# Performance work log

Hardware: AMD Instinct MI355X
Metric: run time of the kernel (lower is better)

The kernel has to match this reference:

```python
import jax, jax.numpy as jnp
import numpy as np

N_NODES = 100000
N_EDGES = 1600000
D_IN, D_HID, D_OUT = 64, 64, 40


def setup_inputs() -> dict:
    key = jax.random.key(0)
    ks = jax.random.split(key, 6)
    x = jax.random.normal(ks[0], (N_NODES, D_IN), dtype=jnp.float32)
    edge_index = jax.random.randint(ks[1], (2, N_EDGES), 0, N_NODES, dtype=jnp.int32)
    # Glorot-ish init for the two GCNConv linear weights
    W1 = jax.random.normal(ks[2], (D_IN, D_HID), dtype=jnp.float32) * (1.0 / np.sqrt(D_IN))
    b1 = jnp.zeros((D_HID,), dtype=jnp.float32)
    W2 = jax.random.normal(ks[3], (D_HID, D_OUT), dtype=jnp.float32) * (1.0 / np.sqrt(D_HID))
    b2 = jnp.zeros((D_OUT,), dtype=jnp.float32)
    return {"x": x, "edge_index": edge_index, "W1": W1, "b1": b1, "W2": W2, "b2": b2}


def reference(x, edge_index, W1, b1, W2, b2):
    N = x.shape[0]
    # GCNConv: add self-loops, symmetric normalization D^{-1/2}(A+I)D^{-1/2}
    loops = jnp.arange(N, dtype=edge_index.dtype)
    row = jnp.concatenate([edge_index[0], loops])  # source nodes (messages gathered here)
    col = jnp.concatenate([edge_index[1], loops])  # target nodes (scatter-add here)
    deg = jax.ops.segment_sum(jnp.ones_like(col, dtype=x.dtype), col, num_segments=N)
    dinv = jnp.where(deg > 0, jax.lax.rsqrt(deg), 0.0)
    norm = dinv[row] * dinv[col]  # [E+N]

    def gcn_conv(h, W, b):
        h = h @ W                                   # [N, d_out]
        msg = h[row] * norm[:, None]                # gather + scale  [E+N, d_out]
        return jax.ops.segment_sum(msg, col, num_segments=N) + b

    h = jax.nn.relu(gcn_conv(x, W1, b1))  # dropout is identity in eval mode
    logits = gcn_conv(h, W2, b2)
    return jax.nn.log_softmax(logits, axis=1)
```

## Files before the change

### kernel.cpp

```cpp
#include <hip/hip_runtime.h>
#include <hip/hip_bf16.h>
#include <math.h>

#define N_NODES 100000
#define N_EDGES 1600000
#define D_IN 64
#define D_HID 64
#define D_OUT 40
#define NBUCK 256
#define BSZ 391
#define BCAP 10240
#define P3_EPB 4096
#define P3_GRID ((N_EDGES + P3_EPB - 1) / P3_EPB)
#define GEMM_GRID ((N_NODES + 63) / 64)
#define AGG_GRID (N_NODES / 8)

typedef __hip_bfloat16 bf16;
typedef __attribute__((ext_vector_type(8))) short short8;
typedef __attribute__((ext_vector_type(4))) float f32x4;

__device__ __forceinline__ float bflo(unsigned int u) {
    union { unsigned int i; float f; } c; c.i = u << 16; return c.f;
}
__device__ __forceinline__ float bfhi(unsigned int u) {
    union { unsigned int i; float f; } c; c.i = u & 0xFFFF0000u; return c.f;
}
__device__ __forceinline__ unsigned short f2b(float f) {
    union { float f; unsigned int u; } c; c.f = f;
    unsigned int u = c.u + 0x7FFFu + ((c.u >> 16) & 1u);
    return (unsigned short)(u >> 16);
}
__device__ __forceinline__ float i8f(unsigned int w, int b) {
    return (float)((int)(w << ((3 - b) * 8)) >> 24);
}
__device__ __forceinline__ unsigned int qpack(float v0, float v1, float v2,
                                              float v3, float qs) {
    int q0 = __float2int_rn(v0 * qs), q1 = __float2int_rn(v1 * qs);
    int q2 = __float2int_rn(v2 * qs), q3 = __float2int_rn(v3 * qs);
    return (unsigned int)(q0 & 255) | ((unsigned int)(q1 & 255) << 8) |
           ((unsigned int)(q2 & 255) << 16) | ((unsigned int)(q3 & 255) << 24);
}

__global__ __launch_bounds__(256) void k_zero(int* __restrict__ p, int n) {
    int i = blockIdx.x * 256 + threadIdx.x;
    if (i < n) p[i] = 0;
}

__global__ __launch_bounds__(256) void k_place(const int* __restrict__ ei,
                                               int* __restrict__ fill_p,
                                               int* __restrict__ part) {
    __shared__ int cnt_l[NBUCK];
    __shared__ int base_l[NBUCK];
    cnt_l[threadIdx.x] = 0;
    __syncthreads();
    int e0 = blockIdx.x * P3_EPB;
    unsigned int meta[16];
#pragma unroll
    for (int k = 0; k < 16; k++) {
        int e = e0 + k * 256 + threadIdx.x;
        if (e < N_EDGES) {
            unsigned int c = (unsigned int)ei[N_EDGES + e];
            unsigned int b = c / 391u;
            unsigned int lc = c - b * 391u;
            unsigned int slot = atomicAdd(&cnt_l[b], 1);
            meta[k] = (b << 21) | (lc << 12) | slot;
        } else meta[k] = 0xFFFFFFFFu;
    }
    __syncthreads();
    int cv = cnt_l[threadIdx.x];
    if (cv) base_l[threadIdx.x] = threadIdx.x * BCAP +
                                  atomicAdd(&fill_p[threadIdx.x * 16], cv);
    __syncthreads();
#pragma unroll
    for (int k = 0; k < 16; k++) {
        if (meta[k] != 0xFFFFFFFFu) {
            int e = e0 + k * 256 + threadIdx.x;
            unsigned int b = meta[k] >> 21;
            unsigned int lc = (meta[k] >> 12) & 0x1FFu;
            unsigned int slot = meta[k] & 0xFFFu;
            unsigned int r = (unsigned int)ei[e];
            part[base_l[b] + slot] = (int)((lc << 17) | r);
        }
    }
}

__global__ __launch_bounds__(256) void k_build(const int* __restrict__ part,
                                               const int* __restrict__ fill_p,
                                               int* __restrict__ start,
                                               int* __restrict__ nkv,
                                               float* __restrict__ dinv,
                                               int* __restrict__ csr) {
    __shared__ int deg_l[392];
    __shared__ int excl_l[392];
    int tid = threadIdx.x;
    int b = blockIdx.x;
    int m = fill_p[b * 16];
    int base = b * BCAP;
    for (int i = tid; i < 392; i += 256) deg_l[i] = 0;
    __syncthreads();
    for (int i = tid; i < m; i += 256)
        atomicAdd(&deg_l[(unsigned int)part[base + i] >> 17], 1);
    __syncthreads();
    if (tid < 64) {
        int carry = 0;
        for (int ch = 0; ch < 7; ch++) {
            int idx = ch * 64 + tid;
            int val = (idx < 392) ? ((deg_l[idx] + 7) & ~7) : 0;
            int incl = val;
#pragma unroll
            for (int off = 1; off < 64; off <<= 1) {
                int u = __shfl_up(incl, off, 64);
                if (tid >= off) incl += u;
            }
            if (idx < 392) excl_l[idx] = carry + incl - val;
            carry += __shfl(incl, 63, 64);
        }
    }
    __syncthreads();
    int v0 = b * BSZ;
    for (int vl = tid; vl < BSZ; vl += 256) {
        int v = v0 + vl;
        if (v < N_NODES) {
            int d = deg_l[vl];
            start[v] = base + excl_l[vl];
            nkv[v] = (d + 7) >> 3;
            dinv[v] = rsqrtf((float)d + 1.0f);
        }
    }
    __syncthreads();
    for (int j = tid; j < 392 * 8; j += 256) {
        int vl = j >> 3, sl = j & 7;
        int d = deg_l[vl];
        int pc = ((d + 7) & ~7) - d;
        if (sl < pc) csr[base + excl_l[vl] + d + sl] = N_NODES;
    }
    __syncthreads();
    for (int i = tid; i < 392; i += 256) deg_l[i] = 0;
    __syncthreads();
    for (int i = tid; i < m; i += 256) {
        unsigned int p = (unsigned int)part[base + i];
        unsigned int lc = p >> 17;
        int s = atomicAdd(&deg_l[lc], 1);
        csr[base + excl_l[lc] + s] = (int)(p & 0x1FFFFu);
    }
}

__global__ __launch_bounds__(256) void k_prep(const float* __restrict__ W1,
                                              const float* __restrict__ W2,
                                              unsigned short* __restrict__ wp1,
                                              unsigned short* __restrict__ wp2,
                                              unsigned int* __restrict__ gb8,
                                              unsigned int* __restrict__ g2q,
                                              float* __restrict__ scale1,
                                              float* __restrict__ scale2) {
    int tid = threadIdx.x;
    if (tid < 16) gb8[(size_t)N_NODES * 16 + tid] = 0;
    else if (tid < 32) g2q[(size_t)N_NODES * 16 + (tid - 16)] = 0;
    else if (tid == 32) { scale1[N_NODES] = 0.f; scale2[N_NODES] = 0.f; }
    for (int i = tid; i < 4096; i += 256) {
        int e = i & 7, lane = (i >> 3) & 63, t = i >> 9;
        int kk = t >> 2, jt = t & 3;
        int row = kk * 32 + (lane >> 4) * 8 + e;
        int col = jt * 16 + (lane & 15);
        wp1[i] = f2b(W1[row * 64 + col]);
    }
    for (int i = tid; i < 3072; i += 256) {
        int e = i & 7, lane = (i >> 3) & 63, t = i >> 9;
        int kk = t / 3, jt = t - kk * 3;
        int row = kk * 32 + (lane >> 4) * 8 + e;
        int col = jt * 16 + (lane & 15);
        wp2[i] = (col < 40) ? f2b(W2[row * 40 + col]) : (unsigned short)0;
    }
}

__global__ __launch_bounds__(256) void k_gemm1m(const float* __restrict__ x,
                                                const short8* __restrict__ wp,
                                                const float* __restrict__ dinv,
                                                unsigned int* __restrict__ gb8,
                                                float* __restrict__ scale1) {
    int lane = threadIdx.x & 63;
    int wid = threadIdx.x >> 6;
    int node0 = (blockIdx.x * 4 + wid) * 16;
    if (node0 >= N_NODES) return;
    int vr = node0 + (lane & 15);
    if (vr >= N_NODES) vr = N_NODES - 1;
    int kg = lane >> 4;
    const float* px = x + (size_t)vr * 64 + kg * 8;
    short8 b0, b1;
    {
        float4 f0 = *(const float4*)px;
        float4 f1 = *(const float4*)(px + 4);
        b0[0] = (short)f2b(f0.x); b0[1] = (short)f2b(f0.y);
        b0[2] = (short)f2b(f0.z); b0[3] = (short)f2b(f0.w);
        b0[4] = (short)f2b(f1.x); b0[5] = (short)f2b(f1.y);
        b0[6] = (short)f2b(f1.z); b0[7] = (short)f2b(f1.w);
        float4 g0 = *(const float4*)(px + 32);
        float4 g1 = *(const float4*)(px + 36);
        b1[0] = (short)f2b(g0.x); b1[1] = (short)f2b(g0.y);
        b1[2] = (short)f2b(g0.z); b1[3] = (short)f2b(g0.w);
        b1[4] = (short)f2b(g1.x); b1[5] = (short)f2b(g1.y);
        b1[6] = (short)f2b(g1.z); b1[7] = (short)f2b(g1.w);
    }
    f32x4 acc[4];
#pragma unroll
    for (int jt = 0; jt < 4; jt++) acc[jt] = (f32x4){0.f, 0.f, 0.f, 0.f};
#pragma unroll
    for (int jt = 0; jt < 4; jt++) {
        acc[jt] = __builtin_amdgcn_mfma_f32_16x16x32_bf16(
            wp[(0 * 4 + jt) * 64 + lane], b0, acc[jt], 0, 0, 0);
        acc[jt] = __builtin_amdgcn_mfma_f32_16x16x32_bf16(
            wp[(1 * 4 + jt) * 64 + lane], b1, acc[jt], 0, 0, 0);
    }
    float d = dinv[vr];
    float mv[4][4];
    float amax = 0.f;
#pragma unroll
    for (int jt = 0; jt < 4; jt++)
#pragma unroll
        for (int i = 0; i < 4; i++) {
            float val = acc[jt][i] * d;
            mv[jt][i] = val;
            amax = fmaxf(amax, fabsf(val));
        }
    amax = fmaxf(amax, __shfl_xor(amax, 16, 64));
    amax = fmaxf(amax, __shfl_xor(amax, 32, 64));
    float qs = (amax > 0.f) ? 127.f / amax : 0.f;
    if (kg == 0) scale1[vr] = amax * (1.f / 127.f);
    unsigned int* gp = gb8 + (size_t)vr * 16 + kg;
#pragma unroll
    for (int jt = 0; jt < 4; jt++)
        gp[jt * 4] = qpack(mv[jt][0], mv[jt][1], mv[jt][2], mv[jt][3], qs);
}

__global__ __launch_bounds__(256) void k_gemm2m(const unsigned short* __restrict__ hb,
                                                const short8* __restrict__ wp,
                                                const float* __restrict__ dinv,
                                                unsigned int* __restrict__ g2q,
                                                float* __restrict__ scale2) {
    int lane = threadIdx.x & 63;
    int wid = threadIdx.x >> 6;
    int node0 = (blockIdx.x * 4 + wid) * 16;
    if (node0 >= N_NODES) return;
    int vr = node0 + (lane & 15);
    if (vr >= N_NODES) vr = N_NODES - 1;
    int kg = lane >> 4;
    const short8* h8 = (const short8*)hb;
    short8 b0 = h8[(size_t)vr * 8 + kg];
    short8 b1 = h8[(size_t)vr * 8 + 4 + kg];
    f32x4 acc[3];
#pragma unroll
    for (int jt = 0; jt < 3; jt++) acc[jt] = (f32x4){0.f, 0.f, 0.f, 0.f};
#pragma unroll
    for (int jt = 0; jt < 3; jt++) {
        acc[jt] = __builtin_amdgcn_mfma_f32_16x16x32_bf16(
            wp[(0 * 3 + jt) * 64 + lane], b0, acc[jt], 0, 0, 0);
        acc[jt] = __builtin_amdgcn_mfma_f32_16x16x32_bf16(
            wp[(1 * 3 + jt) * 64 + lane], b1, acc[jt], 0, 0, 0);
    }
    float d = dinv[vr];
    bool v2 = (kg < 2);
    float mv[3][4];
    float amax = 0.f;
#pragma unroll
    for (int jt = 0; jt < 3; jt++)
#pragma unroll
        for (int i = 0; i < 4; i++) {
            float val = acc[jt][i] * d;
            mv[jt][i] = val;
            if (jt < 2 || v2) amax = fmaxf(amax, fabsf(val));
        }
    amax = fmaxf(amax, __shfl_xor(amax, 16, 64));
    amax = fmaxf(amax, __shfl_xor(amax, 32, 64));
    float qs = (amax > 0.f) ? 127.f / amax : 0.f;
    if (kg == 0) scale2[vr] = amax * (1.f / 127.f);
    unsigned int* gp = g2q + (size_t)vr * 16;
    gp[0 * 4 + kg] = qpack(mv[0][0], mv[0][1], mv[0][2], mv[0][3], qs);
    gp[1 * 4 + kg] = qpack(mv[1][0], mv[1][1], mv[1][2], mv[1][3], qs);
    gp[8 + kg] = v2 ? qpack(mv[2][0], mv[2][1], mv[2][2], mv[2][3], qs) : 0u;
    gp[12 + kg] = 0u;
}

__global__ __launch_bounds__(256) void k_agg1(const int* __restrict__ csr,
                                              const int* __restrict__ start,
                                              const int* __restrict__ nkv,
                                              const unsigned int* __restrict__ gb8,
                                              const float* __restrict__ scale1,
                                              const float* __restrict__ dinv,
                                              const float* __restrict__ b1,
                                              unsigned short* __restrict__ hb) {
    int lane = threadIdx.x & 63;
    int g = lane >> 3;
    int lq = lane & 7;
    int v0 = (blockIdx.x * 4 + (threadIdx.x >> 6)) * 2;
    int v1 = v0 + 1;
    int s0 = start[v0] + g, s1 = start[v1] + g;
    int n0 = nkv[v0], n1 = nkv[v1];
    float a0=0.f,a1=0.f,a2=0.f,a3=0.f,a4=0.f,a5=0.f,a6=0.f,a7=0.f;
    float c0=0.f,c1=0.f,c2=0.f,c3=0.f,c4=0.f,c5=0.f,c6=0.f,c7=0.f;
    if (g == 0) {
        float sA = scale1[v0];
        uint2 uA = *(const uint2*)(gb8 + (size_t)v0 * 16 + lq * 2);
        a0 = fmaf(i8f(uA.x,0), sA, a0); a1 = fmaf(i8f(uA.x,1), sA, a1);
        a2 = fmaf(i8f(uA.x,2), sA, a2); a3 = fmaf(i8f(uA.x,3), sA, a3);
        a4 = fmaf(i8f(uA.y,0), sA, a4); a5 = fmaf(i8f(uA.y,1), sA, a5);
        a6 = fmaf(i8f(uA.y,2), sA, a6); a7 = fmaf(i8f(uA.y,3), sA, a7);
        float sB = scale1[v1];
        uint2 uB = *(const uint2*)(gb8 + (size_t)v1 * 16 + lq * 2);
        c0 = fmaf(i8f(uB.x,0), sB, c0); c1 = fmaf(i8f(uB.x,1), sB, c1);
        c2 = fmaf(i8f(uB.x,2), sB, c2); c3 = fmaf(i8f(uB.x,3), sB, c3);
        c4 = fmaf(i8f(uB.y,0), sB, c4); c5 = fmaf(i8f(uB.y,1), sB, c5);
        c6 = fmaf(i8f(uB.y,2), sB, c6); c7 = fmaf(i8f(uB.y,3), sB, c7);
    }
    int nc = (n0 < n1) ? n0 : n1;
#pragma unroll 2
    for (int k = 0; k < nc; k++) {
        int r0 = csr[s0 + k * 8];
        int r1 = csr[s1 + k * 8];
        float sA = scale1[r0], sB = scale1[r1];
        uint2 uA = *(const uint2*)(gb8 + (size_t)r0 * 16 + lq * 2);
        uint2 uB = *(const uint2*)(gb8 + (size_t)r1 * 16 + lq * 2);
        a0 = fmaf(i8f(uA.x,0), sA, a0); a1 = fmaf(i8f(uA.x,1), sA, a1);
        a2 = fmaf(i8f(uA.x,2), sA, a2); a3 = fmaf(i8f(uA.x,3), sA, a3);
        a4 = fmaf(i8f(uA.y,0), sA, a4); a5 = fmaf(i8f(uA.y,1), sA, a5);
        a6 = fmaf(i8f(uA.y,2), sA, a6); a7 = fmaf(i8f(uA.y,3), sA, a7);
        c0 = fmaf(i8f(uB.x,0), sB, c0); c1 = fmaf(i8f(uB.x,1), sB, c1);
        c2 = fmaf(i8f(uB.x,2), sB, c2); c3 = fmaf(i8f(uB.x,3), sB, c3);
        c4 = fmaf(i8f(uB.y,0), sB, c4); c5 = fmaf(i8f(uB.y,1), sB, c5);
        c6 = fmaf(i8f(uB.y,2), sB, c6); c7 = fmaf(i8f(uB.y,3), sB, c7);
    }
    for (int k = nc; k < n0; k++) {
        int r = csr[s0 + k * 8];
        float sc = scale1[r];
        uint2 u = *(const uint2*)(gb8 + (size_t)r * 16 + lq * 2);
        a0 = fmaf(i8f(u.x,0), sc, a0); a1 = fmaf(i8f(u.x,1), sc, a1);
        a2 = fmaf(i8f(u.x,2), sc, a2); a3 = fmaf(i8f(u.x,3), sc, a3);
        a4 = fmaf(i8f(u.y,0), sc, a4); a5 = fmaf(i8f(u.y,1), sc, a5);
        a6 = fmaf(i8f(u.y,2), sc, a6); a7 = fmaf(i8f(u.y,3), sc, a7);
    }
    for (int k = nc; k < n1; k++) {
        int r = csr[s1 + k * 8];
        float sc = scale1[r];
        uint2 u = *(const uint2*)(gb8 + (size_t)r * 16 + lq * 2);
        c0 = fmaf(i8f(u.x,0), sc, c0); c1 = fmaf(i8f(u.x,1), sc, c1);
        c2 = fmaf(i8f(u.x,2), sc, c2); c3 = fmaf(i8f(u.x,3), sc, c3);
        c4 = fmaf(i8f(u.y,0), sc, c4); c5 = fmaf(i8f(u.y,1), sc, c5);
        c6 = fmaf(i8f(u.y,2), sc, c6); c7 = fmaf(i8f(u.y,3), sc, c7);
    }
#pragma unroll
    for (int o = 8; o < 64; o <<= 1) {
        a0 += __shfl_xor(a0, o, 64); a1 += __shfl_xor(a1, o, 64);
        a2 += __shfl_xor(a2, o, 64); a3 += __shfl_xor(a3, o, 64);
        a4 += __shfl_xor(a4, o, 64); a5 += __shfl_xor(a5, o, 64);
        a6 += __shfl_xor(a6, o, 64); a7 += __shfl_xor(a7, o, 64);
        c0 += __shfl_xor(c0, o, 64); c1 += __shfl_xor(c1, o, 64);
        c2 += __shfl_xor(c2, o, 64); c3 += __shfl_xor(c3, o, 64);
        c4 += __shfl_xor(c4, o, 64); c5 += __shfl_xor(c5, o, 64);
        c6 += __shfl_xor(c6, o, 64); c7 += __shfl_xor(c7, o, 64);
    }
    bool hi = (lane >= 32);
    int v = hi ? v1 : v0;
    float d = dinv[v];
    float e0 = hi ? c0 : a0, e1 = hi ? c1 : a1, e2 = hi ? c2 : a2;
    float e3 = hi ? c3 : a3, e4 = hi ? c4 : a4, e5 = hi ? c5 : a5;
    float e6 = hi ? c6 : a6, e7 = hi ? c7 : a7;
    float4 bb0 = ((const float4*)b1)[lq * 2];
    float4 bb1 = ((const float4*)b1)[lq * 2 + 1];
    float h0 = fmaxf(d * e0 + bb0.x, 0.f), h1 = fmaxf(d * e1 + bb0.y, 0.f);
    float h2 = fmaxf(d * e2 + bb0.z, 0.f), h3 = fmaxf(d * e3 + bb0.w, 0.f);
    float h4 = fmaxf(d * e4 + bb1.x, 0.f), h5 = fmaxf(d * e5 + bb1.y, 0.f);
    float h6 = fmaxf(d * e6 + bb1.z, 0.f), h7 = fmaxf(d * e7 + bb1.w, 0.f);
    if (g == 0 || g == 4) {
        uint4 o;
        o.x = (unsigned int)f2b(h0) | ((unsigned int)f2b(h1) << 16);
        o.y = (unsigned int)f2b(h2) | ((unsigned int)f2b(h3) << 16);
        o.z = (unsigned int)f2b(h4) | ((unsigned int)f2b(h5) << 16);
        o.w = (unsigned int)f2b(h6) | ((unsigned int)f2b(h7) << 16);
        *(uint4*)(hb + (size_t)v * 64 + lq * 8) = o;
    }
}

__global__ __launch_bounds__(256) void k_agg2(const int* __restrict__ csr,
                                              const int* __restrict__ start,
                                              const int* __restrict__ nkv,
                                              const unsigned int* __restrict__ g2q,
                                              const float* __restrict__ scale2,
                                              const float* __restrict__ dinv,
                                              const float* __restrict__ b2v,
                                              float* __restrict__ out) {
    int lane = threadIdx.x & 63;
    int g = lane >> 3;
    int lq = lane & 7;
    int v0 = (blockIdx.x * 4 + (threadIdx.x >> 6)) * 2;
    int v1 = v0 + 1;
    int s0 = start[v0] + g, s1 = start[v1] + g;
    int n0 = nkv[v0], n1 = nkv[v1];
    float a0=0.f,a1=0.f,a2=0.f,a3=0.f,a4=0.f,a5=0.f,a6=0.f,a7=0.f;
    float c0=0.f,c1=0.f,c2=0.f,c3=0.f,c4=0.f,c5=0.f,c6=0.f,c7=0.f;
    if (g == 0) {
        float sA = scale2[v0];
        uint2 uA = *(const uint2*)(g2q + (size_t)v0 * 16 + lq * 2);
        a0 = fmaf(i8f(uA.x,0), sA, a0); a1 = fmaf(i8f(uA.x,1), sA, a1);
        a2 = fmaf(i8f(uA.x,2), sA, a2); a3 = fmaf(i8f(uA.x,3), sA, a3);
        a4 = fmaf(i8f(uA.y,0), sA, a4); a5 = fmaf(i8f(uA.y,1), sA, a5);
        a6 = fmaf(i8f(uA.y,2), sA, a6); a7 = fmaf(i8f(uA.y,3), sA, a7);
        float sB = scale2[v1];
        uint2 uB = *(const uint2*)(g2q + (size_t)v1 * 16 + lq * 2);
        c0 = fmaf(i8f(uB.x,0), sB, c0); c1 = fmaf(i8f(uB.x,1), sB, c1);
        c2 = fmaf(i8f(uB.x,2), sB, c2); c3 = fmaf(i8f(uB.x,3), sB, c3);
        c4 = fmaf(i8f(uB.y,0), sB, c4); c5 = fmaf(i8f(uB.y,1), sB, c5);
        c6 = fmaf(i8f(uB.y,2), sB, c6); c7 = fmaf(i8f(uB.y,3), sB, c7);
    }
    int nc = (n0 < n1) ? n0 : n1;
#pragma unroll 2
    for (int k = 0; k < nc; k++) {
        int r0 = csr[s0 + k * 8];
        int r1 = csr[s1 + k * 8];
        float sA = scale2[r0], sB = scale2[r1];
        uint2 uA = *(const uint2*)(g2q + (size_t)r0 * 16 + lq * 2);
        uint2 uB = *(const uint2*)(g2q + (size_t)r1 * 16 + lq * 2);
        a0 = fmaf(i8f(uA.x,0), sA, a0); a1 = fmaf(i8f(uA.x,1), sA, a1);
        a2 = fmaf(i8f(uA.x,2), sA, a2); a3 = fmaf(i8f(uA.x,3), sA, a3);
        a4 = fmaf(i8f(uA.y,0), sA, a4); a5 = fmaf(i8f(uA.y,1), sA, a5);
        a6 = fmaf(i8f(uA.y,2), sA, a6); a7 = fmaf(i8f(uA.y,3), sA, a7);
        c0 = fmaf(i8f(uB.x,0), sB, c0); c1 = fmaf(i8f(uB.x,1), sB, c1);
        c2 = fmaf(i8f(uB.x,2), sB, c2); c3 = fmaf(i8f(uB.x,3), sB, c3);
        c4 = fmaf(i8f(uB.y,0), sB, c4); c5 = fmaf(i8f(uB.y,1), sB, c5);
        c6 = fmaf(i8f(uB.y,2), sB, c6); c7 = fmaf(i8f(uB.y,3), sB, c7);
    }
    for (int k = nc; k < n0; k++) {
        int r = csr[s0 + k * 8];
        float sc = scale2[r];
        uint2 u = *(const uint2*)(g2q + (size_t)r * 16 + lq * 2);
        a0 = fmaf(i8f(u.x,0), sc, a0); a1 = fmaf(i8f(u.x,1), sc, a1);
        a2 = fmaf(i8f(u.x,2), sc, a2); a3 = fmaf(i8f(u.x,3), sc, a3);
        a4 = fmaf(i8f(u.y,0), sc, a4); a5 = fmaf(i8f(u.y,1), sc, a5);
        a6 = fmaf(i8f(u.y,2), sc, a6); a7 = fmaf(i8f(u.y,3), sc, a7);
    }
    for (int k = nc; k < n1; k++) {
        int r = csr[s1 + k * 8];
        float sc = scale2[r];
        uint2 u = *(const uint2*)(g2q + (size_t)r * 16 + lq * 2);
        c0 = fmaf(i8f(u.x,0), sc, c0); c1 = fmaf(i8f(u.x,1), sc, c1);
        c2 = fmaf(i8f(u.x,2), sc, c2); c3 = fmaf(i8f(u.x,3), sc, c3);
        c4 = fmaf(i8f(u.y,0), sc, c4); c5 = fmaf(i8f(u.y,1), sc, c5);
        c6 = fmaf(i8f(u.y,2), sc, c6); c7 = fmaf(i8f(u.y,3), sc, c7);
    }
#pragma unroll
    for (int o = 8; o < 64; o <<= 1) {
        a0 += __shfl_xor(a0, o, 64); a1 += __shfl_xor(a1, o, 64);
        a2 += __shfl_xor(a2, o, 64); a3 += __shfl_xor(a3, o, 64);
        a4 += __shfl_xor(a4, o, 64); a5 += __shfl_xor(a5, o, 64);
        a6 += __shfl_xor(a6, o, 64); a7 += __shfl_xor(a7, o, 64);
        c0 += __shfl_xor(c0, o, 64); c1 += __shfl_xor(c1, o, 64);
        c2 += __shfl_xor(c2, o, 64); c3 += __shfl_xor(c3, o, 64);
        c4 += __shfl_xor(c4, o, 64); c5 += __shfl_xor(c5, o, 64);
        c6 += __shfl_xor(c6, o, 64); c7 += __shfl_xor(c7, o, 64);
    }
    bool hi = (lane >= 32);
    int v = hi ? v1 : v0;
    float d = dinv[v];
    float e0 = hi ? c0 : a0, e1 = hi ? c1 : a1, e2 = hi ? c2 : a2;
    float e3 = hi ? c3 : a3, e4 = hi ? c4 : a4, e5 = hi ? c5 : a5;
    float e6 = hi ? c6 : a6, e7 = hi ? c7 : a7;
    bool act = (lq < 5);
    float4 bb0 = act ? ((const float4*)b2v)[lq * 2] : make_float4(0.f,0.f,0.f,0.f);
    float4 bb1 = act ? ((const float4*)b2v)[lq * 2 + 1] : make_float4(0.f,0.f,0.f,0.f);
    float l0 = act ? d * e0 + bb0.x : -INFINITY;
    float l1 = act ? d * e1 + bb0.y : -INFINITY;
    float l2 = act ? d * e2 + bb0.z : -INFINITY;
    float l3 = act ? d * e3 + bb0.w : -INFINITY;
    float l4 = act ? d * e4 + bb1.x : -INFINITY;
    float l5 = act ? d * e5 + bb1.y : -INFINITY;
    float l6 = act ? d * e6 + bb1.z : -INFINITY;
    float l7 = act ? d * e7 + bb1.w : -INFINITY;
    float m = fmaxf(fmaxf(fmaxf(l0, l1), fmaxf(l2, l3)),
                    fmaxf(fmaxf(l4, l5), fmaxf(l6, l7)));
#pragma unroll
    for (int o = 1; o < 8; o <<= 1) m = fmaxf(m, __shfl_xor(m, o, 64));
    float ex = act ? (__expf(l0 - m) + __expf(l1 - m) + __expf(l2 - m) +
                      __expf(l3 - m) + __expf(l4 - m) + __expf(l5 - m) +
                      __expf(l6 - m) + __expf(l7 - m)) : 0.f;
#pragma unroll
    for (int o = 1; o < 8; o <<= 1) ex += __shfl_xor(ex, o, 64);
    float lse = m + logf(ex);
    if ((g == 0 || g == 4) && act) {
        float* op = out + (size_t)v * 40 + lq * 8;
        *(float4*)op = make_float4(l0 - lse, l1 - lse, l2 - lse, l3 - lse);
        *(float4*)(op + 4) = make_float4(l4 - lse, l5 - lse, l6 - lse, l7 - lse);
    }
}

extern "C" void kernel_launch(void* const* d_in, const int* in_sizes, int n_in,
                              void* d_out, int out_size, void* d_ws, size_t ws_size,
                              hipStream_t stream) {
    const float* x  = (const float*)d_in[0];
    const int*   ei = (const int*)d_in[1];
    const float* W1 = (const float*)d_in[2];
    const float* b1 = (const float*)d_in[3];
    const float* W2 = (const float*)d_in[4];
    const float* b2 = (const float*)d_in[5];
    float* out = (float*)d_out;

    const int N = N_NODES;
    int*   part  = (int*)d_ws;
    int*   csr   = part + NBUCK * BCAP;
    int*   start = csr + NBUCK * BCAP;
    int*   nkv   = start + N;
    int*   fill  = nkv + N;
    float* dinv  = (float*)(fill + 4096);
    float* scale1 = dinv + N;
    float* scale2 = scale1 + N + 4;
    unsigned short* hb  = (unsigned short*)(scale2 + N + 4);
    unsigned int* gb8 = (unsigned int*)(hb + (size_t)N * 64);
    unsigned int* g2q = gb8 + (size_t)(N + 1) * 16;
    unsigned short* wp1 = (unsigned short*)(g2q + (size_t)(N + 1) * 16);
    unsigned short* wp2 = wp1 + 4096;

    k_zero<<<16, 256, 0, stream>>>(fill, 4096);
    k_prep<<<1, 256, 0, stream>>>(W1, W2, wp1, wp2, gb8, g2q, scale1, scale2);
    k_place<<<P3_GRID, 256, 0, stream>>>(ei, fill, part);
    k_build<<<NBUCK, 256, 0, stream>>>(part, fill, start, nkv, dinv, csr);
    k_gemm1m<<<GEMM_GRID, 256, 0, stream>>>(x, (const short8*)wp1, dinv, gb8, scale1);
    k_agg1<<<AGG_GRID, 256, 0, stream>>>(csr, start, nkv, gb8, scale1, dinv, b1, hb);
    k_gemm2m<<<GEMM_GRID, 256, 0, stream>>>(hb, (const short8*)wp2, dinv, g2q, scale2);
    k_agg2<<<AGG_GRID, 256, 0, stream>>>(csr, start, nkv, g2q, scale2, dinv, b2, out);
}
```

Baseline: 239.7 us.

## Replace per-node int8 quantized messages with fp16 messages in aggregation

Switches the gathered per-node feature buffers from int8 with a per-node float scale to packed fp16 values. Aggregation now accumulates them with fdot2 instead of sign-extend plus fma, which drops the separate scale lookups and the amax reduction in the GEMM epilogues. The cost is twice the bytes per gathered row (128B for layer 1, 80B for layer 2), so the random gathers move more traffic. The bucket capacity is also reduced, shrinking the workspace.

```diff
diff --git a/kernel.cpp b/kernel.cpp
--- a/kernel.cpp
+++ b/kernel.cpp
@@ -9,7 +9,7 @@
 #define D_OUT 40
 #define NBUCK 256
 #define BSZ 391
-#define BCAP 10240
+#define BCAP 8192
 #define P3_EPB 4096
 #define P3_GRID ((N_EDGES + P3_EPB - 1) / P3_EPB)
 #define GEMM_GRID ((N_NODES + 63) / 64)
@@ -18,27 +18,32 @@
 typedef __hip_bfloat16 bf16;
 typedef __attribute__((ext_vector_type(8))) short short8;
 typedef __attribute__((ext_vector_type(4))) float f32x4;
-
-__device__ __forceinline__ float bflo(unsigned int u) {
-    union { unsigned int i; float f; } c; c.i = u << 16; return c.f;
-}
-__device__ __forceinline__ float bfhi(unsigned int u) {
-    union { unsigned int i; float f; } c; c.i = u & 0xFFFF0000u; return c.f;
-}
+typedef __attribute__((ext_vector_type(2))) _Float16 h2f;
+typedef __attribute__((ext_vector_type(2))) __fp16 fp16x2;
+
 __device__ __forceinline__ unsigned short f2b(float f) {
     union { float f; unsigned int u; } c; c.f = f;
     unsigned int u = c.u + 0x7FFFu + ((c.u >> 16) & 1u);
     return (unsigned short)(u >> 16);
 }
-__device__ __forceinline__ float i8f(unsigned int w, int b) {
-    return (float)((int)(w << ((3 - b) * 8)) >> 24);
-}
-__device__ __forceinline__ unsigned int qpack(float v0, float v1, float v2,
-                                              float v3, float qs) {
-    int q0 = __float2int_rn(v0 * qs), q1 = __float2int_rn(v1 * qs);
-    int q2 = __float2int_rn(v2 * qs), q3 = __float2int_rn(v3 * qs);
-    return (unsigned int)(q0 & 255) | ((unsigned int)(q1 & 255) << 8) |
-           ((unsigned int)(q2 & 255) << 16) | ((unsigned int)(q3 & 255) << 24);
+__device__ __forceinline__ unsigned int pkh(float a, float b) {
+#if __has_builtin(__builtin_amdgcn_cvt_pkrtz)
+    union { fp16x2 h; unsigned int u; } c;
+    c.h = __builtin_amdgcn_cvt_pkrtz(a, b);
+    return c.u;
+#else
+    union { _Float16 h[2]; unsigned int u; } c;
+    c.h[0] = (_Float16)a; c.h[1] = (_Float16)b; return c.u;
+#endif
+}
+__device__ __forceinline__ void acc2(unsigned int w, float& e, float& o) {
+    union { unsigned int u; h2f h; } c; c.u = w;
+#if __has_builtin(__builtin_amdgcn_fdot2)
+    e = __builtin_amdgcn_fdot2(c.h, (h2f){(_Float16)1.f, (_Float16)0.f}, e, false);
+    o = __builtin_amdgcn_fdot2(c.h, (h2f){(_Float16)0.f, (_Float16)1.f}, o, false);
+#else
+    e += (float)c.h[0]; o += (float)c.h[1];
+#endif
 }
 
 __global__ __launch_bounds__(256) void k_zero(int* __restrict__ p, int n) {
@@ -149,14 +154,11 @@
                                               const float* __restrict__ W2,
                                               unsigned short* __restrict__ wp1,
                                               unsigned short* __restrict__ wp2,
-                                              unsigned int* __restrict__ gb8,
-                                              unsigned int* __restrict__ g2q,
-                                              float* __restrict__ scale1,
-                                              float* __restrict__ scale2) {
+                                              unsigned int* __restrict__ gbh,
+                                              unsigned int* __restrict__ g2h) {
     int tid = threadIdx.x;
-    if (tid < 16) gb8[(size_t)N_NODES * 16 + tid] = 0;
-    else if (tid < 32) g2q[(size_t)N_NODES * 16 + (tid - 16)] = 0;
-    else if (tid == 32) { scale1[N_NODES] = 0.f; scale2[N_NODES] = 0.f; }
+    if (tid < 32) gbh[(size_t)N_NODES * 32 + tid] = 0;
+    else if (tid < 52) g2h[(size_t)N_NODES * 20 + (tid - 32)] = 0;
     for (int i = tid; i < 4096; i += 256) {
         int e = i & 7, lane = (i >> 3) & 63, t = i >> 9;
         int kk = t >> 2, jt = t & 3;
@@ -176,8 +178,7 @@
 __global__ __launch_bounds__(256) void k_gemm1m(const float* __restrict__ x,
                                                 const short8* __restrict__ wp,
                                                 const float* __restrict__ dinv,
-                                                unsigned int* __restrict__ gb8,
-                                                float* __restrict__ scale1) {
+                                                unsigned short* __restrict__ gbh) {
     int lane = threadIdx.x & 63;
     int wid = threadIdx.x >> 6;
     int node0 = (blockIdx.x * 4 + wid) * 16;
@@ -212,31 +213,20 @@
             wp[(1 * 4 + jt) * 64 + lane], b1, acc[jt], 0, 0, 0);
     }
     float d = dinv[vr];
-    float mv[4][4];
-    float amax = 0.f;
-#pragma unroll
-    for (int jt = 0; jt < 4; jt++)
-#pragma unroll
-        for (int i = 0; i < 4; i++) {
-            float val = acc[jt][i] * d;
-            mv[jt][i] = val;
-            amax = fmaxf(amax, fabsf(val));
-        }
-    amax = fmaxf(amax, __shfl_xor(amax, 16, 64));
-    amax = fmaxf(amax, __shfl_xor(amax, 32, 64));
-    float qs = (amax > 0.f) ? 127.f / amax : 0.f;
-    if (kg == 0) scale1[vr] = amax * (1.f / 127.f);
-    unsigned int* gp = gb8 + (size_t)vr * 16 + kg;
-#pragma unroll
-    for (int jt = 0; jt < 4; jt++)
-        gp[jt * 4] = qpack(mv[jt][0], mv[jt][1], mv[jt][2], mv[jt][3], qs);
+    unsigned short* gp = gbh + (size_t)vr * 64 + kg * 4;
+#pragma unroll
+    for (int jt = 0; jt < 4; jt++) {
+        uint2 w;
+        w.x = pkh(acc[jt][0] * d, acc[jt][1] * d);
+        w.y = pkh(acc[jt][2] * d, acc[jt][3] * d);
+        *(uint2*)(gp + jt * 16) = w;
+    }
 }
 
 __global__ __launch_bounds__(256) void k_gemm2m(const unsigned short* __restrict__ hb,
                                                 const short8* __restrict__ wp,
                                                 const float* __restrict__ dinv,
-                                                unsigned int* __restrict__ g2q,
-                                                float* __restrict__ scale2) {
+                                                unsigned short* __restrict__ g2h) {
     int lane = threadIdx.x & 63;
     int wid = threadIdx.x >> 6;
     int node0 = (blockIdx.x * 4 + wid) * 16;
@@ -258,33 +248,26 @@
             wp[(1 * 3 + jt) * 64 + lane], b1, acc[jt], 0, 0, 0);
     }
     float d = dinv[vr];
-    bool v2 = (kg < 2);
-    float mv[3][4];
-    float amax = 0.f;
-#pragma unroll
-    for (int jt = 0; jt < 3; jt++)
-#pragma unroll
-        for (int i = 0; i < 4; i++) {
-            float val = acc[jt][i] * d;
-            mv[jt][i] = val;
-            if (jt < 2 || v2) amax = fmaxf(amax, fabsf(val));
-        }
-    amax = fmaxf(amax, __shfl_xor(amax, 16, 64));
-    amax = fmaxf(amax, __shfl_xor(amax, 32, 64));
-    float qs = (amax > 0.f) ? 127.f / amax : 0.f;
-    if (kg == 0) scale2[vr] = amax * (1.f / 127.f);
-    unsigned int* gp = g2q + (size_t)vr * 16;
-    gp[0 * 4 + kg] = qpack(mv[0][0], mv[0][1], mv[0][2], mv[0][3], qs);
-    gp[1 * 4 + kg] = qpack(mv[1][0], mv[1][1], mv[1][2], mv[1][3], qs);
-    gp[8 + kg] = v2 ? qpack(mv[2][0], mv[2][1], mv[2][2], mv[2][3], qs) : 0u;
-    gp[12 + kg] = 0u;
+    unsigned short* gp = g2h + (size_t)vr * 40;
+#pragma unroll
+    for (int jt = 0; jt < 2; jt++) {
+        uint2 w;
+        w.x = pkh(acc[jt][0] * d, acc[jt][1] * d);
+        w.y = pkh(acc[jt][2] * d, acc[jt][3] * d);
+        *(uint2*)(gp + jt * 16 + kg * 4) = w;
+    }
+    if (kg < 2) {
+        uint2 w;
+        w.x = pkh(acc[2][0] * d, acc[2][1] * d);
+        w.y = pkh(acc[2][2] * d, acc[2][3] * d);
+        *(uint2*)(gp + 32 + kg * 4) = w;
+    }
 }
 
 __global__ __launch_bounds__(256) void k_agg1(const int* __restrict__ csr,
                                               const int* __restrict__ start,
                                               const int* __restrict__ nkv,
-                                              const unsigned int* __restrict__ gb8,
-                                              const float* __restrict__ scale1,
+                                              const unsigned int* __restrict__ gbh,
                                               const float* __restrict__ dinv,
                                               const float* __restrict__ b1,
                                               unsigned short* __restrict__ hb) {
@@ -298,53 +281,36 @@
     float a0=0.f,a1=0.f,a2=0.f,a3=0.f,a4=0.f,a5=0.f,a6=0.f,a7=0.f;
     float c0=0.f,c1=0.f,c2=0.f,c3=0.f,c4=0.f,c5=0.f,c6=0.f,c7=0.f;
     if (g == 0) {
-        float sA = scale1[v0];
-        uint2 uA = *(const uint2*)(gb8 + (size_t)v0 * 16 + lq * 2);
-        a0 = fmaf(i8f(uA.x,0), sA, a0); a1 = fmaf(i8f(uA.x,1), sA, a1);
-        a2 = fmaf(i8f(uA.x,2), sA, a2); a3 = fmaf(i8f(uA.x,3), sA, a3);
-        a4 = fmaf(i8f(uA.y,0), sA, a4); a5 = fmaf(i8f(uA.y,1), sA, a5);
-        a6 = fmaf(i8f(uA.y,2), sA, a6); a7 = fmaf(i8f(uA.y,3), sA, a7);
-        float sB = scale1[v1];
-        uint2 uB = *(const uint2*)(gb8 + (size_t)v1 * 16 + lq * 2);
-        c0 = fmaf(i8f(uB.x,0), sB, c0); c1 = fmaf(i8f(uB.x,1), sB, c1);
-        c2 = fmaf(i8f(uB.x,2), sB, c2); c3 = fmaf(i8f(uB.x,3), sB, c3);
-        c4 = fmaf(i8f(uB.y,0), sB, c4); c5 = fmaf(i8f(uB.y,1), sB, c5);
-        c6 = fmaf(i8f(uB.y,2), sB, c6); c7 = fmaf(i8f(uB.y,3), sB, c7);
+        uint4 uA = *(const uint4*)(gbh + (size_t)v0 * 32 + lq * 4);
+        acc2(uA.x, a0, a1); acc2(uA.y, a2, a3);
+        acc2(uA.z, a4, a5); acc2(uA.w, a6, a7);
+        uint4 uB = *(const uint4*)(gbh + (size_t)v1 * 32 + lq * 4);
+        acc2(uB.x, c0, c1); acc2(uB.y, c2, c3);
+        acc2(uB.z, c4, c5); acc2(uB.w, c6, c7);
     }
     int nc = (n0 < n1) ? n0 : n1;
 #pragma unroll 2
     for (int k = 0; k < nc; k++) {
         int r0 = csr[s0 + k * 8];
         int r1 = csr[s1 + k * 8];
-        float sA = scale1[r0], sB = scale1[r1];
-        uint2 uA = *(const uint2*)(gb8 + (size_t)r0 * 16 + lq * 2);
-        uint2 uB = *(const uint2*)(gb8 + (size_t)r1 * 16 + lq * 2);
-        a0 = fmaf(i8f(uA.x,0), sA, a0); a1 = fmaf(i8f(uA.x,1), sA, a1);
-        a2 = fmaf(i8f(uA.x,2), sA, a2); a3 = fmaf(i8f(uA.x,3), sA, a3);
-        a4 = fmaf(i8f(uA.y,0), sA, a4); a5 = fmaf(i8f(uA.y,1), sA, a5);
-        a6 = fmaf(i8f(uA.y,2), sA, a6); a7 = fmaf(i8f(uA.y,3), sA, a7);
-        c0 = fmaf(i8f(uB.x,0), sB, c0); c1 = fmaf(i8f(uB.x,1), sB, c1);
-        c2 = fmaf(i8f(uB.x,2), sB, c2); c3 = fmaf(i8f(uB.x,3), sB, c3);
-        c4 = fmaf(i8f(uB.y,0), sB, c4); c5 = fmaf(i8f(uB.y,1), sB, c5);
-        c6 = fmaf(i8f(uB.y,2), sB, c6); c7 = fmaf(i8f(uB.y,3), sB, c7);
+        uint4 uA = *(const uint4*)(gbh + (size_t)r0 * 32 + lq * 4);
+        uint4 uB = *(const uint4*)(gbh + (size_t)r1 * 32 + lq * 4);
+        acc2(uA.x, a0, a1); acc2(uA.y, a2, a3);
+        acc2(uA.z, a4, a5); acc2(uA.w, a6, a7);
+        acc2(uB.x, c0, c1); acc2(uB.y, c2, c3);
+        acc2(uB.z, c4, c5); acc2(uB.w, c6, c7);
     }
     for (int k = nc; k < n0; k++) {
         int r = csr[s0 + k * 8];
-        float sc = scale1[r];
-        uint2 u = *(const uint2*)(gb8 + (size_t)r * 16 + lq * 2);
-        a0 = fmaf(i8f(u.x,0), sc, a0); a1 = fmaf(i8f(u.x,1), sc, a1);
-        a2 = fmaf(i8f(u.x,2), sc, a2); a3 = fmaf(i8f(u.x,3), sc, a3);
-        a4 = fmaf(i8f(u.y,0), sc, a4); a5 = fmaf(i8f(u.y,1), sc, a5);
-        a6 = fmaf(i8f(u.y,2), sc, a6); a7 = fmaf(i8f(u.y,3), sc, a7);
+        uint4 u = *(const uint4*)(gbh + (size_t)r * 32 + lq * 4);
+        acc2(u.x, a0, a1); acc2(u.y, a2, a3);
+        acc2(u.z, a4, a5); acc2(u.w, a6, a7);
     }
     for (int k = nc; k < n1; k++) {
         int r = csr[s1 + k * 8];
-        float sc = scale1[r];
-        uint2 u = *(const uint2*)(gb8 + (size_t)r * 16 + lq * 2);
-        c0 = fmaf(i8f(u.x,0), sc, c0); c1 = fmaf(i8f(u.x,1), sc, c1);
-        c2 = fmaf(i8f(u.x,2), sc, c2); c3 = fmaf(i8f(u.x,3), sc, c3);
-        c4 = fmaf(i8f(u.y,0), sc, c4); c5 = fmaf(i8f(u.y,1), sc, c5);
-        c6 = fmaf(i8f(u.y,2), sc, c6); c7 = fmaf(i8f(u.y,3), sc, c7);
+        uint4 u = *(const uint4*)(gbh + (size_t)r * 32 + lq * 4);
+        acc2(u.x, c0, c1); acc2(u.y, c2, c3);
+        acc2(u.z, c4, c5); acc2(u.w, c6, c7);
     }
 #pragma unroll
     for (int o = 8; o < 64; o <<= 1) {
@@ -382,14 +348,14 @@
 __global__ __launch_bounds__(256) void k_agg2(const int* __restrict__ csr,
                                               const int* __restrict__ start,
                                               const int* __restrict__ nkv,
-                                              const unsigned int* __restrict__ g2q,
-                                              const float* __restrict__ scale2,
+                                              const unsigned int* __restrict__ g2h,
                                               const float* __restrict__ dinv,
                                               const float* __restrict__ b2v,
                                               float* __restrict__ out) {
     int lane = threadIdx.x & 63;
     int g = lane >> 3;
     int lq = lane & 7;
+    int lqc = (lq < 5) ? lq : 0;
     int v0 = (blockIdx.x * 4 + (threadIdx.x >> 6)) * 2;
     int v1 = v0 + 1;
     int s0 = start[v0] + g, s1 = start[v1] + g;
@@ -397,53 +363,36 @@
     float a0=0.f,a1=0.f,a2=0.f,a3=0.f,a4=0.f,a5=0.f,a6=0.f,a7=0.f;
     float c0=0.f,c1=0.f,c2=0.f,c3=0.f,c4=0.f,c5=0.f,c6=0.f,c7=0.f;
     if (g == 0) {
-        float sA = scale2[v0];
-        uint2 uA = *(const uint2*)(g2q + (size_t)v0 * 16 + lq * 2);
-        a0 = fmaf(i8f(uA.x,0), sA, a0); a1 = fmaf(i8f(uA.x,1), sA, a1);
-        a2 = fmaf(i8f(uA.x,2), sA, a2); a3 = fmaf(i8f(uA.x,3), sA, a3);
-        a4 = fmaf(i8f(uA.y,0), sA, a4); a5 = fmaf(i8f(uA.y,1), sA, a5);
-        a6 = fmaf(i8f(uA.y,2), sA, a6); a7 = fmaf(i8f(uA.y,3), sA, a7);
-        float sB = scale2[v1];
-        uint2 uB = *(const uint2*)(g2q + (size_t)v1 * 16 + lq * 2);
-        c0 = fmaf(i8f(uB.x,0), sB, c0); c1 = fmaf(i8f(uB.x,1), sB, c1);
-        c2 = fmaf(i8f(uB.x,2), sB, c2); c3 = fmaf(i8f(uB.x,3), sB, c3);
-        c4 = fmaf(i8f(uB.y,0), sB, c4); c5 = fmaf(i8f(uB.y,1), sB, c5);
-        c6 = fmaf(i8f(uB.y,2), sB, c6); c7 = fmaf(i8f(uB.y,3), sB, c7);
+        uint4 uA = *(const uint4*)(g2h + (size_t)v0 * 20 + lqc * 4);
+        acc2(uA.x, a0, a1); acc2(uA.y, a2, a3);
+        acc2(uA.z, a4, a5); acc2(uA.w, a6, a7);
+        uint4 uB = *(const uint4*)(g2h + (size_t)v1 * 20 + lqc * 4);
+        acc2(uB.x, c0, c1); acc2(uB.y, c2, c3);
+        acc2(uB.z, c4, c5); acc2(uB.w, c6, c7);
     }
     int nc = (n0 < n1) ? n0 : n1;
 #pragma unroll 2
     for (int k = 0; k < nc; k++) {
         int r0 = csr[s0 + k * 8];
         int r1 = csr[s1 + k * 8];
-        float sA = scale2[r0], sB = scale2[r1];
-        uint2 uA = *(const uint2*)(g2q + (size_t)r0 * 16 + lq * 2);
-        uint2 uB = *(const uint2*)(g2q + (size_t)r1 * 16 + lq * 2);
-        a0 = fmaf(i8f(uA.x,0), sA, a0); a1 = fmaf(i8f(uA.x,1), sA, a1);
-        a2 = fmaf(i8f(uA.x,2), sA, a2); a3 = fmaf(i8f(uA.x,3), sA, a3);
-        a4 = fmaf(i8f(uA.y,0), sA, a4); a5 = fmaf(i8f(uA.y,1), sA, a5);
-        a6 = fmaf(i8f(uA.y,2), sA, a6); a7 = fmaf(i8f(uA.y,3), sA, a7);
-        c0 = fmaf(i8f(uB.x,0), sB, c0); c1 = fmaf(i8f(uB.x,1), sB, c1);
-        c2 = fmaf(i8f(uB.x,2), sB, c2); c3 = fmaf(i8f(uB.x,3), sB, c3);
-        c4 = fmaf(i8f(uB.y,0), sB, c4); c5 = fmaf(i8f(uB.y,1), sB, c5);
-        c6 = fmaf(i8f(uB.y,2), sB, c6); c7 = fmaf(i8f(uB.y,3), sB, c7);
+        uint4 uA = *(const uint4*)(g2h + (size_t)r0 * 20 + lqc * 4);
+        uint4 uB = *(const uint4*)(g2h + (size_t)r1 * 20 + lqc * 4);
+        acc2(uA.x, a0, a1); acc2(uA.y, a2, a3);
+        acc2(uA.z, a4, a5); acc2(uA.w, a6, a7);
+        acc2(uB.x, c0, c1); acc2(uB.y, c2, c3);
+        acc2(uB.z, c4, c5); acc2(uB.w, c6, c7);
     }
     for (int k = nc; k < n0; k++) {
         int r = csr[s0 + k * 8];
-        float sc = scale2[r];
-        uint2 u = *(const uint2*)(g2q + (size_t)r * 16 + lq * 2);
-        a0 = fmaf(i8f(u.x,0), sc, a0); a1 = fmaf(i8f(u.x,1), sc, a1);
-        a2 = fmaf(i8f(u.x,2), sc, a2); a3 = fmaf(i8f(u.x,3), sc, a3);
-        a4 = fmaf(i8f(u.y,0), sc, a4); a5 = fmaf(i8f(u.y,1), sc, a5);
-        a6 = fmaf(i8f(u.y,2), sc, a6); a7 = fmaf(i8f(u.y,3), sc, a7);
+        uint4 u = *(const uint4*)(g2h + (size_t)r * 20 + lqc * 4);
+        acc2(u.x, a0, a1); acc2(u.y, a2, a3);
+        acc2(u.z, a4, a5); acc2(u.w, a6, a7);
     }
     for (int k = nc; k < n1; k++) {
         int r = csr[s1 + k * 8];
-        float sc = scale2[r];
-        uint2 u = *(const uint2*)(g2q + (size_t)r * 16 + lq * 2);
-        c0 = fmaf(i8f(u.x,0), sc, c0); c1 = fmaf(i8f(u.x,1), sc, c1);
-        c2 = fmaf(i8f(u.x,2), sc, c2); c3 = fmaf(i8f(u.x,3), sc, c3);
-        c4 = fmaf(i8f(u.y,0), sc, c4); c5 = fmaf(i8f(u.y,1), sc, c5);
-        c6 = fmaf(i8f(u.y,2), sc, c6); c7 = fmaf(i8f(u.y,3), sc, c7);
+        uint4 u = *(const uint4*)(g2h + (size_t)r * 20 + lqc * 4);
+        acc2(u.x, c0, c1); acc2(u.y, c2, c3);
+        acc2(u.z, c4, c5); acc2(u.w, c6, c7);
     }
 #pragma unroll
     for (int o = 8; o < 64; o <<= 1) {
@@ -508,20 +457,21 @@
     int*   nkv   = start + N;
     int*   fill  = nkv + N;
     float* dinv  = (float*)(fill + 4096);
-    float* scale1 = dinv + N;
-    float* scale2 = scale1 + N + 4;
-    unsigned short* hb  = (unsigned short*)(scale2 + N + 4);
-    unsigned int* gb8 = (unsigned int*)(hb + (size_t)N * 64);
-    unsigned int* g2q = gb8 + (size_t)(N + 1) * 16;
-    unsigned short* wp1 = (unsigned short*)(g2q + (size_t)(N + 1) * 16);
+    unsigned short* hb  = (unsigned short*)(dinv + N);
+    unsigned short* gbh = hb + (size_t)N * 64;
+    unsigned short* g2h = gbh + (size_t)(N + 1) * 64;
+    unsigned short* wp1 = g2h + (size_t)(N + 1) * 40;
     unsigned short* wp2 = wp1 + 4096;
 
     k_zero<<<16, 256, 0, stream>>>(fill, 4096);
-    k_prep<<<1, 256, 0, stream>>>(W1, W2, wp1, wp2, gb8, g2q, scale1, scale2);
+    k_prep<<<1, 256, 0, stream>>>(W1, W2, wp1, wp2,
+                                  (unsigned int*)gbh, (unsigned int*)g2h);
     k_place<<<P3_GRID, 256, 0, stream>>>(ei, fill, part);
     k_build<<<NBUCK, 256, 0, stream>>>(part, fill, start, nkv, dinv, csr);
-    k_gemm1m<<<GEMM_GRID, 256, 0, stream>>>(x, (const short8*)wp1, dinv, gb8, scale1);
-    k_agg1<<<AGG_GRID, 256, 0, stream>>>(csr, start, nkv, gb8, scale1, dinv, b1, hb);
-    k_gemm2m<<<GEMM_GRID, 256, 0, stream>>>(hb, (const short8*)wp2, dinv, g2q, scale2);
-    k_agg2<<<AGG_GRID, 256, 0, stream>>>(csr, start, nkv, g2q, scale2, dinv, b2, out);
-}
+    k_gemm1m<<<GEMM_GRID, 256, 0, stream>>>(x, (const short8*)wp1, dinv, gbh);
+    k_agg1<<<AGG_GRID, 256, 0, stream>>>(csr, start, nkv, (const unsigned int*)gbh,
+                                         dinv, b1, hb);
+    k_gemm2m<<<GEMM_GRID, 256, 0, stream>>>(hb, (const short8*)wp2, dinv, g2h);
+    k_agg2<<<AGG_GRID, 256, 0, stream>>>(csr, start, nkv, (const unsigned int*)g2h,
+                                         dinv, b2, out);
+}
```

New measurement: 215.9 us, median of 2. -9.9%, faster.
